# Performance work log

Hardware: AMD Instinct MI355X
Metric: run time of the kernel (lower is better)

Reference implementation:

```python
import jax, jax.numpy as jnp
import numpy as np

N_BASIS = 16
CUTOFF = 5.0
S3 = 3.0 ** 0.5


def _cg_121():
    # Real Clebsch-Gordan for 1o x 2e -> 1o built from the equivariant map
    # (v, T) -> T @ v where T is the traceless symmetric matrix encoded by the
    # 5 real l=2 components (e3nn y-principal convention). Normalized to unit
    # Frobenius norm (wigner-3j-like normalization).
    s15 = np.sqrt(15.0); s5 = np.sqrt(5.0)
    C = np.zeros((3, 3, 5))
    for j in range(5):
        c = np.zeros(5); c[j] = 1.0
        T = np.zeros((3, 3))
        T[0, 2] = T[2, 0] = c[0] / s15
        T[0, 1] = T[1, 0] = c[1] / s15
        T[1, 2] = T[2, 1] = c[3] / s15
        Tyy = 2.0 * c[2] / (3.0 * s5)
        T[1, 1] = Tyy
        T[2, 2] = -Tyy / 2.0 + c[4] / s15
        T[0, 0] = -Tyy / 2.0 - c[4] / s15
        C[:, :, j] = T
    C /= np.linalg.norm(C)
    return jnp.asarray(C, dtype=jnp.float32)


def _sph(n):
    # component-normalized real spherical harmonics l=0,1,2 of unit vectors n [E,3]
    x, y, z = n[:, 0], n[:, 1], n[:, 2]
    Y0 = jnp.ones_like(x)
    Y1 = S3 * n  # [E,3]
    s15 = 15.0 ** 0.5; s5 = 5.0 ** 0.5
    Y2 = jnp.stack([s15 * x * z, s15 * x * y, 0.5 * s5 * (3 * y * y - 1.0),
                    s15 * y * z, 0.5 * s15 * (z * z - x * x)], axis=-1)  # [E,5]
    return Y0, Y1, Y2


def _tfn_forward(x, pos, W1, W2, edge_index, cg121):
    row, col = edge_index[0], edge_index[1]
    E = row.shape[0]
    N = pos.shape[0]
    ev = pos[row] - pos[col]                         # [E,3]
    d = jnp.sqrt(jnp.sum(ev * ev, axis=-1) + 1e-12)  # [E]
    n = ev / d[:, None]
    # Gaussian radial basis, 16 centers on [0, cutoff]
    mu = jnp.linspace(0.0, CUTOFF, N_BASIS)
    delta = CUTOFF / (N_BASIS - 1)
    rbf = jnp.exp(-((d[:, None] - mu) ** 2) / (2.0 * delta * delta))  # [E,16]
    # normalized 2-layer MLP -> per-edge TP weights [E, 576]
    h = jax.nn.relu((rbf @ W1) / jnp.sqrt(16.0))
    w = (h @ W2) / jnp.sqrt(64.0)
    Y0, Y1, Y2 = _sph(n)
    ss = jnp.stack([Y0, Y0], axis=-1)   # [E,2]  2x0e
    sv = jnp.stack([Y1, Y1], axis=1)    # [E,2,3] 2x1o
    st = Y2                              # [E,5]  1x2e
    xs = x[row, :8]                      # [E,8]  8x0e
    xv = x[row, 8:].reshape(E, 8, 3)     # [E,8,3] 8x1o
    wA = w[:, 0:128].reshape(E, 8, 2, 8)
    wB = w[:, 128:256].reshape(E, 8, 2, 8)
    wC = w[:, 256:384].reshape(E, 8, 2, 8)
    wD = w[:, 384:512].reshape(E, 8, 2, 8)
    wE = w[:, 512:576].reshape(E, 8, 8)
    a0 = 1.0 / jnp.sqrt(32.0)            # sqrt(2*0+1)/sqrt(fan_in=32)
    a1 = jnp.sqrt(3.0) / jnp.sqrt(40.0)  # sqrt(2*1+1)/sqrt(fan_in=40)
    out_s = a0 * (jnp.einsum('euvw,eu,ev->ew', wA, xs, ss)
                  + jnp.einsum('euvw,eui,evi->ew', wB, xv, sv) / S3)
    out_v = a1 * (jnp.einsum('euvw,eu,evk->ewk', wC, xs, sv) / S3
                  + jnp.einsum('euvw,euk,ev->ewk', wD, xv, ss) / S3
                  + jnp.einsum('euw,eui,ej,kij->ewk', wE, xv, st, cg121))
    out = jnp.concatenate([out_s, out_v.reshape(E, 24)], axis=-1)  # [E,32]
    y = jax.ops.segment_sum(out, row, num_segments=N)              # [N,32]
    # gate: silu on scalar (l=0) channels only
    return jnp.concatenate([jax.nn.silu(y[:, :8]), y[:, 8:]], axis=-1)


def setup_inputs() -> dict:
    key = jax.random.key(0)
    k1, k2, k3, k4, k5 = jax.random.split(key, 5)
    N, E = 25000, 400000
    x = jax.random.normal(k1, (N, 32), dtype=jnp.float32)
    pos = jax.random.normal(k2, (N, 3), dtype=jnp.float32)
    edge_index = jax.random.randint(k3, (2, E), 0, N, dtype=jnp.int64 if jax.config.read('jax_enable_x64') else jnp.int32)
    W1 = jax.random.normal(k4, (16, 64), dtype=jnp.float32)
    W2 = jax.random.normal(k5, (64, 576), dtype=jnp.float32)
    return {"x": x, "pos": pos, "edge_index": edge_index, "W1": W1, "W2": W2}


def reference(x, pos, edge_index, W1, W2):
    cg121 = _cg_121()
    return _tfn_forward(x, pos, W1, W2, edge_index, cg121)
```

## Files before the change

kernel.cpp:

```cpp
#include <hip/hip_runtime.h>
#include <hip/hip_fp16.h>


#define INV_S3  0.5773502691896258f
#define A0S     0.1767766952966369f
#define A1S     0.27386127875258306f
#define S15     3.872983346207417f
#define S5      2.23606797749979f
#define INV_S10 0.31622776601683794f
#define INV_S30 0.18257418583505536f

#define TBL   2048
#define DMAX  8.0f
#define CAP   64

typedef _Float16 half8 __attribute__((ext_vector_type(8)));
typedef _Float16 half2v __attribute__((ext_vector_type(2)));

__global__ __launch_bounds__(256) void prep_all(
    const float* __restrict__ W1, const float* __restrict__ W2,
    const int* __restrict__ ei, const float* __restrict__ pos,
    _Float16* __restrict__ T, int* __restrict__ cnt,
    float4* __restrict__ srec, int E) {

    __shared__ float hs[4][64];
    int tid = threadIdx.x;
    int wv = tid >> 6, lane = tid & 63;
    int j = blockIdx.x * 4 + wv;

    float hv = 0.f;
    if (j < TBL) {
        float d = (float)j * (DMAX / (float)(TBL - 1));
        float acc = 0.f;
#pragma unroll
        for (int i = 0; i < 16; ++i) {
            float t = d - (float)i * (1.0f / 3.0f);
            float r = __expf(-4.5f * t * t);
            acc = fmaf(r, W1[i * 64 + lane], acc);
        }
        hv = fmaxf(acc, 0.f) * 0.25f;
    }
    if (j < TBL || blockIdx.x < TBL / 4) hs[wv][lane] = hv;
    __syncthreads();

    if (j < TBL) {
        int u = lane >> 3, wo = lane & 7;
        int b0 = u * 16 + wo;
        int b4 = 512 + u * 8 + wo;
        float a0 = 0.f, a1 = 0.f, a2 = 0.f, a3 = 0.f, a4 = 0.f;
#pragma unroll 4
        for (int k = 0; k < 64; ++k) {
            float hk = hs[wv][k];
            const float* Wk = W2 + k * 576;
            a0 = fmaf(hk, Wk[b0]       + Wk[b0 + 8],       a0);
            a1 = fmaf(hk, Wk[128 + b0] + Wk[128 + b0 + 8], a1);
            a2 = fmaf(hk, Wk[256 + b0] + Wk[256 + b0 + 8], a2);
            a3 = fmaf(hk, Wk[384 + b0] + Wk[384 + b0 + 8], a3);
            a4 = fmaf(hk, Wk[b4], a4);
        }
        _Float16* Tr = T + (size_t)j * 320;
        int base = u * 16 + wo * 2;
        Tr[base]           = (_Float16)a0;
        Tr[base + 1]       = (_Float16)a1;
        Tr[128 + base]     = (_Float16)a2;
        Tr[128 + base + 1] = (_Float16)a3;
        Tr[256 + u * 8 + wo] = (_Float16)a4;
    }

    int gtid = blockIdx.x * 256 + tid;
    int gsz = gridDim.x * 256;
    for (int e = gtid; e < E; e += gsz) {
        int row = ei[e];
        int col = ei[E + e];
        float ax = pos[3 * row + 0] - pos[3 * col + 0];
        float ay = pos[3 * row + 1] - pos[3 * col + 1];
        float az = pos[3 * row + 2] - pos[3 * col + 2];
        float d2 = ax * ax + ay * ay + az * az + 1e-12f;
        float invd = rsqrtf(d2);
        float dd = d2 * invd;
        int p = atomicAdd(&cnt[row], 1);
        if (p < CAP) {
            float4 r;
            r.x = ax * invd;
            r.y = ay * invd;
            r.z = az * invd;
            r.w = dd;
            srec[(size_t)row * CAP + p] = r;
        }
    }
}

__global__ __launch_bounds__(256) void tfn_node(
    const float* __restrict__ x, const float4* __restrict__ srec,
    const int* __restrict__ cnt, const _Float16* __restrict__ T,
    float* __restrict__ y, int N) {

    int wv = threadIdx.x >> 6, lane = threadIdx.x & 63;
    int n = blockIdx.x * 4 + wv;
    if (n >= N) return;

    int g = lane >> 3;
    int u = lane & 7;
    int kc = cnt[n];
    if (kc > CAP) kc = CAP;
    const float4* recs = srec + (size_t)n * CAP;

    const float* xr = x + (size_t)n * 32;
    float xu  = xr[u];
    float xv0 = xr[8 + 3 * u + 0];
    float xv1 = xr[8 + 3 * u + 1];
    float xv2 = xr[8 + 3 * u + 2];
    _Float16 xuh = (_Float16)xu;
    _Float16 p30 = (_Float16)(xv0 * INV_S3);
    _Float16 p31 = (_Float16)(xv1 * INV_S3);
    _Float16 p32 = (_Float16)(xv2 * INV_S3);

    float V[32];
#pragma unroll
    for (int z = 0; z < 32; ++z) V[z] = 0.f;

    int rounds = (kc + 7) >> 3;
    float4 rec = make_float4(0.f, 0.f, 0.f, 0.f);
    if (rounds > 0) rec = recs[g];
    for (int rd = 0; rd < rounds; ++rd) {
        float4 cur = rec;
        int slot = rd * 8 + g;
        if (rd + 1 < rounds) rec = recs[slot + 8];
        if (slot < kc) {
            float nx = cur.x, ny = cur.y, nz = cur.z;
            float dd = cur.w;

            float fj = dd * ((float)(TBL - 1) / DMAX);
            int j0 = (int)fj;
            j0 = min(j0, TBL - 2);
            float tf = fminf(fj - (float)j0, 1.0f);
            _Float16 th = (_Float16)tf;

            const _Float16* Ar = T + (size_t)j0 * 320;
            const _Float16* Au = Ar + u * 16;
            half8 A01a = *(const half8*)(Au);
            half8 A01b = *(const half8*)(Au + 8);
            half8 A23a = *(const half8*)(Au + 128);
            half8 A23b = *(const half8*)(Au + 136);
            half8 A4   = *(const half8*)(Ar + 256 + u * 8);
            half8 B01a = *(const half8*)(Au + 320);
            half8 B01b = *(const half8*)(Au + 328);
            half8 B23a = *(const half8*)(Au + 448);
            half8 B23b = *(const half8*)(Au + 456);
            half8 B4   = *(const half8*)(Ar + 576 + u * 8);

            float qu = xv0 * nx + xv1 * ny + xv2 * nz;
            float Y22 = 0.5f * S5 * (3.f * ny * ny - 1.f);
            float Y24 = 0.5f * S15 * (nz * nz - nx * nx);
            float M00 = -Y22 * INV_S30 - Y24 * INV_S10;
            float M11 = 2.f * Y22 * INV_S30;
            float M22 = -Y22 * INV_S30 + Y24 * INV_S10;
            float M01 = (S15 * nx * ny) * INV_S10;
            float M02 = (S15 * nx * nz) * INV_S10;
            float M12 = (S15 * ny * nz) * INV_S10;
            float m0 = M00 * xv0 + M01 * xv1 + M02 * xv2;
            float m1 = M01 * xv0 + M11 * xv1 + M12 * xv2;
            float m2 = M02 * xv0 + M12 * xv1 + M22 * xv2;

            half2v xq;  xq.x = xuh;  xq.y = (_Float16)qu;
            half2v c0;  c0.x = (_Float16)(xu * nx);  c0.y = p30;
            half2v c1;  c1.x = (_Float16)(xu * ny);  c1.y = p31;
            half2v c2;  c2.x = (_Float16)(xu * nz);  c2.y = p32;

            half8 w01a, w01b, w23a, w23b, w4l;
#pragma unroll
            for (int z = 0; z < 8; ++z) {
                w01a[z] = A01a[z] + (B01a[z] - A01a[z]) * th;
                w01b[z] = A01b[z] + (B01b[z] - A01b[z]) * th;
                w23a[z] = A23a[z] + (B23a[z] - A23a[z]) * th;
                w23b[z] = A23b[z] + (B23b[z] - A23b[z]) * th;
                w4l[z]  = A4[z]   + (B4[z]   - A4[z])   * th;
            }

#pragma unroll
            for (int z = 0; z < 4; ++z) {
                half2v pa; pa.x = w01a[2 * z]; pa.y = w01a[2 * z + 1];
                V[z] = __builtin_amdgcn_fdot2(pa, xq, V[z], false);
                half2v pb; pb.x = w01b[2 * z]; pb.y = w01b[2 * z + 1];
                V[4 + z] = __builtin_amdgcn_fdot2(pb, xq, V[4 + z], false);
            }

#pragma unroll
            for (int z = 0; z < 4; ++z) {
                half2v pa; pa.x = w23a[2 * z]; pa.y = w23a[2 * z + 1];
                int b = 8 + 3 * z;
                V[b]     = __builtin_amdgcn_fdot2(pa, c0, V[b],     false);
                V[b + 1] = __builtin_amdgcn_fdot2(pa, c1, V[b + 1], false);
                V[b + 2] = __builtin_amdgcn_fdot2(pa, c2, V[b + 2], false);
                half2v pb; pb.x = w23b[2 * z]; pb.y = w23b[2 * z + 1];
                int b2 = 8 + 3 * (z + 4);
                V[b2]     = __builtin_amdgcn_fdot2(pb, c0, V[b2],     false);
                V[b2 + 1] = __builtin_amdgcn_fdot2(pb, c1, V[b2 + 1], false);
                V[b2 + 2] = __builtin_amdgcn_fdot2(pb, c2, V[b2 + 2], false);
            }

#pragma unroll
            for (int z = 0; z < 8; ++z) {
                float we = (float)w4l[z];
                V[8 + 3 * z]  = fmaf(m0, we, V[8 + 3 * z]);
                V[9 + 3 * z]  = fmaf(m1, we, V[9 + 3 * z]);
                V[10 + 3 * z] = fmaf(m2, we, V[10 + 3 * z]);
            }
        }
    }

#pragma unroll
    for (int h = 16; h >= 1; h >>= 1) {
        bool hi = (lane & h) != 0;
#pragma unroll
        for (int k = 0; k < h; ++k) {
            float lo = V[k], up = V[k + h];
            float keep = hi ? up : lo;
            float send = hi ? lo : up;
            V[k] = keep + __shfl_xor(send, h, 64);
        }
    }
    V[0] += __shfl_xor(V[0], 32, 64);

    if (lane < 32) {
        float v = V[0] * 0.125f * (lane < 8 ? A0S : A1S);
        if (lane < 8) v = v / (1.0f + __expf(-v));
        y[(size_t)n * 32 + lane] = v;
    }
}

extern "C" void kernel_launch(void* const* d_in, const int* in_sizes, int n_in,
                              void* d_out, int out_size, void* d_ws, size_t ws_size,
                              hipStream_t stream) {
    const float* x   = (const float*)d_in[0];
    const float* pos = (const float*)d_in[1];
    const int*   ei  = (const int*)d_in[2];
    const float* W1  = (const float*)d_in[3];
    const float* W2  = (const float*)d_in[4];
    int N = in_sizes[1] / 3;
    int E = in_sizes[2] / 2;

    char* ws = (char*)d_ws;
    size_t off = 0;
    _Float16* T    = (_Float16*)(ws + off); off += (size_t)TBL * 320 * 2;
    int*      cnt  = (int*)(ws + off);      off += (size_t)N * 4;
    float4*   srec = (float4*)(ws + off);   off += (size_t)N * CAP * 16;

    float* y = (float*)d_out;

    hipMemsetAsync(cnt, 0, (size_t)N * 4, stream);
    hipLaunchKernelGGL(prep_all, dim3(2048), dim3(256), 0, stream,
                       W1, W2, ei, pos, T, cnt, srec, E);
    hipLaunchKernelGGL(tfn_node, dim3((N + 3) / 4), dim3(256), 0, stream,
                       x, srec, cnt, T, y, N);
}
```

Baseline: 142.9 us.

## Double-buffer table row loads across edge rounds in node kernel

```diff
diff --git a/kernel.cpp b/kernel.cpp
--- a/kernel.cpp
+++ b/kernel.cpp
@@ -40,7 +40,7 @@
         }
         hv = fmaxf(acc, 0.f) * 0.25f;
     }
-    if (j < TBL || blockIdx.x < TBL / 4) hs[wv][lane] = hv;
+    hs[wv][lane] = hv;
     __syncthreads();
 
     if (j < TBL) {
@@ -90,6 +90,23 @@
     }
 }
 
+
+#define LOADT(J, T01a, T01b, T23a, T23b, T4, U01a, U01b, U23a, U23b, U4)   \
+    {                                                                      \
+        const _Float16* Ar_ = T + (size_t)(J) * 320;                       \
+        const _Float16* Au_ = Ar_ + u * 16;                                \
+        T01a = *(const half8*)(Au_);                                       \
+        T01b = *(const half8*)(Au_ + 8);                                   \
+        T23a = *(const half8*)(Au_ + 128);                                 \
+        T23b = *(const half8*)(Au_ + 136);                                 \
+        T4   = *(const half8*)(Ar_ + 256 + u * 8);                         \
+        U01a = *(const half8*)(Au_ + 320);                                 \
+        U01b = *(const half8*)(Au_ + 328);                                 \
+        U23a = *(const half8*)(Au_ + 448);                                 \
+        U23b = *(const half8*)(Au_ + 456);                                 \
+        U4   = *(const half8*)(Ar_ + 576 + u * 8);                         \
+    }
+
 __global__ __launch_bounds__(256) void tfn_node(
     const float* __restrict__ x, const float4* __restrict__ srec,
     const int* __restrict__ cnt, const _Float16* __restrict__ T,
@@ -119,92 +136,113 @@
 #pragma unroll
     for (int z = 0; z < 32; ++z) V[z] = 0.f;
 
+#define COMPUTE(CUR, SLOT, J0, A01a, A01b, A23a, A23b, A4, B01a, B01b, B23a, B23b, B4) \
+    if ((SLOT) < kc) {                                                     \
+        float nx = (CUR).x, ny = (CUR).y, nz = (CUR).z;                    \
+        float fj = (CUR).w * ((float)(TBL - 1) / DMAX);                    \
+        float tf = fminf(fj - (float)(J0), 1.0f);                          \
+        _Float16 th = (_Float16)tf;                                        \
+        float qu = xv0 * nx + xv1 * ny + xv2 * nz;                         \
+        float Y22 = 0.5f * S5 * (3.f * ny * ny - 1.f);                     \
+        float Y24 = 0.5f * S15 * (nz * nz - nx * nx);                      \
+        float M00 = -Y22 * INV_S30 - Y24 * INV_S10;                        \
+        float M11 = 2.f * Y22 * INV_S30;                                   \
+        float M22 = -Y22 * INV_S30 + Y24 * INV_S10;                        \
+        float M01 = (S15 * nx * ny) * INV_S10;                             \
+        float M02 = (S15 * nx * nz) * INV_S10;                             \
+        float M12 = (S15 * ny * nz) * INV_S10;                             \
+        float m0 = M00 * xv0 + M01 * xv1 + M02 * xv2;                      \
+        float m1 = M01 * xv0 + M11 * xv1 + M12 * xv2;                      \
+        float m2 = M02 * xv0 + M12 * xv1 + M22 * xv2;                      \
+        half2v xq;  xq.x = xuh;  xq.y = (_Float16)qu;                      \
+        half2v c0;  c0.x = (_Float16)(xu * nx);  c0.y = p30;               \
+        half2v c1;  c1.x = (_Float16)(xu * ny);  c1.y = p31;               \
+        half2v c2;  c2.x = (_Float16)(xu * nz);  c2.y = p32;               \
+        half8 w01a, w01b, w23a, w23b, w4l;                                 \
+        _Pragma("unroll")                                                  \
+        for (int z = 0; z < 8; ++z) {                                      \
+            w01a[z] = A01a[z] + (B01a[z] - A01a[z]) * th;                  \
+            w01b[z] = A01b[z] + (B01b[z] - A01b[z]) * th;                  \
+            w23a[z] = A23a[z] + (B23a[z] - A23a[z]) * th;                  \
+            w23b[z] = A23b[z] + (B23b[z] - A23b[z]) * th;                  \
+            w4l[z]  = A4[z]   + (B4[z]   - A4[z])   * th;                  \
+        }                                                                  \
+        _Pragma("unroll")                                                  \
+        for (int z = 0; z < 4; ++z) {                                      \
+            half2v pa; pa.x = w01a[2 * z]; pa.y = w01a[2 * z + 1];         \
+            V[z] = __builtin_amdgcn_fdot2(pa, xq, V[z], false);            \
+            half2v pb; pb.x = w01b[2 * z]; pb.y = w01b[2 * z + 1];         \
+            V[4 + z] = __builtin_amdgcn_fdot2(pb, xq, V[4 + z], false);    \
+        }                                                                  \
+        _Pragma("unroll")                                                  \
+        for (int z = 0; z < 4; ++z) {                                      \
+            half2v pa; pa.x = w23a[2 * z]; pa.y = w23a[2 * z + 1];         \
+            int b = 8 + 3 * z;                                             \
+            V[b]     = __builtin_amdgcn_fdot2(pa, c0, V[b],     false);    \
+            V[b + 1] = __builtin_amdgcn_fdot2(pa, c1, V[b + 1], false);    \
+            V[b + 2] = __builtin_amdgcn_fdot2(pa, c2, V[b + 2], false);    \
+            half2v pb; pb.x = w23b[2 * z]; pb.y = w23b[2 * z + 1];         \
+            int b2 = 8 + 3 * (z + 4);                                      \
+            V[b2]     = __builtin_amdgcn_fdot2(pb, c0, V[b2],     false);  \
+            V[b2 + 1] = __builtin_amdgcn_fdot2(pb, c1, V[b2 + 1], false);  \
+            V[b2 + 2] = __builtin_amdgcn_fdot2(pb, c2, V[b2 + 2], false);  \
+        }                                                                  \
+        _Pragma("unroll")                                                  \
+        for (int z = 0; z < 8; ++z) {                                      \
+            float we = (float)w4l[z];                                      \
+            V[8 + 3 * z]  = fmaf(m0, we, V[8 + 3 * z]);                    \
+            V[9 + 3 * z]  = fmaf(m1, we, V[9 + 3 * z]);                    \
+            V[10 + 3 * z] = fmaf(m2, we, V[10 + 3 * z]);                   \
+        }                                                                  \
+    }
+
     int rounds = (kc + 7) >> 3;
-    float4 rec = make_float4(0.f, 0.f, 0.f, 0.f);
-    if (rounds > 0) rec = recs[g];
-    for (int rd = 0; rd < rounds; ++rd) {
-        float4 cur = rec;
-        int slot = rd * 8 + g;
-        if (rd + 1 < rounds) rec = recs[slot + 8];
-        if (slot < kc) {
-            float nx = cur.x, ny = cur.y, nz = cur.z;
-            float dd = cur.w;
-
-            float fj = dd * ((float)(TBL - 1) / DMAX);
-            int j0 = (int)fj;
-            j0 = min(j0, TBL - 2);
-            float tf = fminf(fj - (float)j0, 1.0f);
-            _Float16 th = (_Float16)tf;
-
-            const _Float16* Ar = T + (size_t)j0 * 320;
-            const _Float16* Au = Ar + u * 16;
-            half8 A01a = *(const half8*)(Au);
-            half8 A01b = *(const half8*)(Au + 8);
-            half8 A23a = *(const half8*)(Au + 128);
-            half8 A23b = *(const half8*)(Au + 136);
-            half8 A4   = *(const half8*)(Ar + 256 + u * 8);
-            half8 B01a = *(const half8*)(Au + 320);
-            half8 B01b = *(const half8*)(Au + 328);
-            half8 B23a = *(const half8*)(Au + 448);
-            half8 B23b = *(const half8*)(Au + 456);
-            half8 B4   = *(const half8*)(Ar + 576 + u * 8);
-
-            float qu = xv0 * nx + xv1 * ny + xv2 * nz;
-            float Y22 = 0.5f * S5 * (3.f * ny * ny - 1.f);
-            float Y24 = 0.5f * S15 * (nz * nz - nx * nx);
-            float M00 = -Y22 * INV_S30 - Y24 * INV_S10;
-            float M11 = 2.f * Y22 * INV_S30;
-            float M22 = -Y22 * INV_S30 + Y24 * INV_S10;
-            float M01 = (S15 * nx * ny) * INV_S10;
-            float M02 = (S15 * nx * nz) * INV_S10;
-            float M12 = (S15 * ny * nz) * INV_S10;
-            float m0 = M00 * xv0 + M01 * xv1 + M02 * xv2;
-            float m1 = M01 * xv0 + M11 * xv1 + M12 * xv2;
-            float m2 = M02 * xv0 + M12 * xv1 + M22 * xv2;
-
-            half2v xq;  xq.x = xuh;  xq.y = (_Float16)qu;
-            half2v c0;  c0.x = (_Float16)(xu * nx);  c0.y = p30;
-            half2v c1;  c1.x = (_Float16)(xu * ny);  c1.y = p31;
-            half2v c2;  c2.x = (_Float16)(xu * nz);  c2.y = p32;
-
-            half8 w01a, w01b, w23a, w23b, w4l;
-#pragma unroll
-            for (int z = 0; z < 8; ++z) {
-                w01a[z] = A01a[z] + (B01a[z] - A01a[z]) * th;
-                w01b[z] = A01b[z] + (B01b[z] - A01b[z]) * th;
-                w23a[z] = A23a[z] + (B23a[z] - A23a[z]) * th;
-                w23b[z] = A23b[z] + (B23b[z] - A23b[z]) * th;
-                w4l[z]  = A4[z]   + (B4[z]   - A4[z])   * th;
+    if (rounds > 0) {
+        float4 rA = recs[g];
+        float fjA = rA.w * ((float)(TBL - 1) / DMAX);
+        int jA = max(min((int)fjA, TBL - 2), 0);
+        half8 tA01a, tA01b, tA23a, tA23b, tA4, uA01a, uA01b, uA23a, uA23b, uA4;
+        LOADT(jA, tA01a, tA01b, tA23a, tA23b, tA4, uA01a, uA01b, uA23a, uA23b, uA4);
+
+        float4 rB = rA; int jB = 0;
+        half8 tB01a, tB01b, tB23a, tB23b, tB4, uB01a, uB01b, uB23a, uB23b, uB4;
+        if (rounds > 1) {
+            rB = recs[8 + g];
+            float fjB = rB.w * ((float)(TBL - 1) / DMAX);
+            jB = max(min((int)fjB, TBL - 2), 0);
+            LOADT(jB, tB01a, tB01b, tB23a, tB23b, tB4, uB01a, uB01b, uB23a, uB23b, uB4);
+        }
+
+        for (int rd = 0; rd < rounds; rd += 2) {
+            {
+                float4 rN = rA;
+                bool haveN = (rd + 2 < rounds);
+                if (haveN) rN = recs[(rd + 2) * 8 + g];
+                COMPUTE(rA, rd * 8 + g, jA,
+                        tA01a, tA01b, tA23a, tA23b, tA4,
+                        uA01a, uA01b, uA23a, uA23b, uA4);
+                if (haveN) {
+                    rA = rN;
+                    float fjN = rA.w * ((float)(TBL - 1) / DMAX);
+                    jA = max(min((int)fjN, TBL - 2), 0);
+                    LOADT(jA, tA01a, tA01b, tA23a, tA23b, tA4,
+                              uA01a, uA01b, uA23a, uA23b, uA4);
+                }
             }
-
-#pragma unroll
-            for (int z = 0; z < 4; ++z) {
-                half2v pa; pa.x = w01a[2 * z]; pa.y = w01a[2 * z + 1];
-                V[z] = __builtin_amdgcn_fdot2(pa, xq, V[z], false);
-                half2v pb; pb.x = w01b[2 * z]; pb.y = w01b[2 * z + 1];
-                V[4 + z] = __builtin_amdgcn_fdot2(pb, xq, V[4 + z], false);
-            }
-
-#pragma unroll
-            for (int z = 0; z < 4; ++z) {
-                half2v pa; pa.x = w23a[2 * z]; pa.y = w23a[2 * z + 1];
-                int b = 8 + 3 * z;
-                V[b]     = __builtin_amdgcn_fdot2(pa, c0, V[b],     false);
-                V[b + 1] = __builtin_amdgcn_fdot2(pa, c1, V[b + 1], false);
-                V[b + 2] = __builtin_amdgcn_fdot2(pa, c2, V[b + 2], false);
-                half2v pb; pb.x = w23b[2 * z]; pb.y = w23b[2 * z + 1];
-                int b2 = 8 + 3 * (z + 4);
-                V[b2]     = __builtin_amdgcn_fdot2(pb, c0, V[b2],     false);
-                V[b2 + 1] = __builtin_amdgcn_fdot2(pb, c1, V[b2 + 1], false);
-                V[b2 + 2] = __builtin_amdgcn_fdot2(pb, c2, V[b2 + 2], false);
-            }
-
-#pragma unroll
-            for (int z = 0; z < 8; ++z) {
-                float we = (float)w4l[z];
-                V[8 + 3 * z]  = fmaf(m0, we, V[8 + 3 * z]);
-                V[9 + 3 * z]  = fmaf(m1, we, V[9 + 3 * z]);
-                V[10 + 3 * z] = fmaf(m2, we, V[10 + 3 * z]);
+            if (rd + 1 < rounds) {
+                float4 rM = rB;
+                bool haveM = (rd + 3 < rounds);
+                if (haveM) rM = recs[(rd + 3) * 8 + g];
+                COMPUTE(rB, (rd + 1) * 8 + g, jB,
+                        tB01a, tB01b, tB23a, tB23b, tB4,
+                        uB01a, uB01b, uB23a, uB23b, uB4);
+                if (haveM) {
+                    rB = rM;
+                    float fjM = rB.w * ((float)(TBL - 1) / DMAX);
+                    jB = max(min((int)fjM, TBL - 2), 0);
+                    LOADT(jB, tB01a, tB01b, tB23a, tB23b, tB4,
+                              uB01a, uB01b, uB23a, uB23b, uB4);
+                }
             }
         }
     }
```

Result: slower. 151.1 us (+5.7%).
